# Performance work log

Hardware: AMD Instinct MI355X
Metric: run time of the kernel (lower is better)

## Reference

```python
import jax, jax.numpy as jnp
import numpy as np

N = 50000; E = 800000; IN_DIM = 128; HID = 128; OUT = 128; K_TARGET = 5000


def setup_inputs() -> dict:
    key = jax.random.key(0)
    ks = jax.random.split(key, 7)
    x = jax.random.normal(ks[0], (N, IN_DIM), jnp.float32)
    edge_index = jax.random.randint(ks[1], (2, E), 0, N, dtype=jnp.int32)
    W1 = jax.random.normal(ks[2], (IN_DIM, HID), jnp.float32) / np.float32(np.sqrt(IN_DIM))
    b1 = jnp.zeros((HID,), jnp.float32)
    W2 = jax.random.normal(ks[3], (HID, OUT), jnp.float32) / np.float32(np.sqrt(HID))
    b2 = jnp.zeros((OUT,), jnp.float32)
    w_score = jax.random.normal(ks[4], (HID,), jnp.float32) / np.float32(np.sqrt(HID))
    W_skip = jax.random.normal(ks[5], (HID, OUT), jnp.float32) / np.float32(np.sqrt(HID))
    b_skip = jnp.zeros((OUT,), jnp.float32)
    return dict(x=x, edge_index=edge_index, W1=W1, b1=b1, W2=W2, b2=b2,
                w_score=w_score, W_skip=W_skip, b_skip=b_skip)


def _gcn(h_in, row, col, W, b, nseg, edge_w=None):
    # PyG GCNConv with add_self_loops=True, normalize=True:
    # deg[i] = sum of incoming edge weights at col + 1 (self loop, weight 1)
    h = h_in @ W
    w = edge_w if edge_w is not None else jnp.ones(row.shape, h.dtype)
    deg = jax.ops.segment_sum(w, col, num_segments=nseg) + 1.0
    dinv = jax.lax.rsqrt(deg)
    norm = dinv[row] * w * dinv[col]                     # [E]
    agg = jax.ops.segment_sum(norm[:, None] * h[row], col, num_segments=nseg)
    agg = agg + (dinv * dinv)[:, None] * h               # self-loop messages
    return agg + b


def _forward(x, edge_index, W1, b1, W2, b2, w_score, W_skip, b_skip):
    row, col = edge_index[0], edge_index[1]
    n = x.shape[0]
    e = row.shape[0]
    x1 = jax.nn.relu(_gcn(x, row, col, W1, b1, n))       # conv1 + relu (dropout: eval mode)
    raw = x1 @ w_score                                    # [N]
    x1g = x1 * jnp.tanh(raw)[:, None]                     # gated features
    K = min(K_TARGET, n)
    _, kept = jax.lax.top_k(raw, K)                       # sorted desc, ties -> lower index
    keep_mask = jnp.zeros((n,), bool).at[kept].set(True)
    deg = jax.ops.segment_sum(jnp.ones((e,), jnp.int32), row, num_segments=n)  # bincount(row)
    # neighbor insertion order: edge i appends col[i] to neigh[row[i]] (order 2i),
    # then row[i] to neigh[col[i]] (order 2i+1)
    owners = jnp.concatenate([row, col])
    neighs = jnp.concatenate([col, row])
    e_ar = jnp.arange(e, dtype=jnp.int32)
    order = jnp.concatenate([2 * e_ar, 2 * e_ar + 1])
    M = 2 * e + 2
    valid = keep_mask[neighs]
    comp = deg[neighs] * M + (M - 1 - order)
    comp = jnp.where(valid, comp, -1)
    best = jax.ops.segment_max(comp, owners, num_segments=n)
    has_valid = best >= 0
    is_best = valid & (comp == best[owners])              # unique per owner (order unique)
    best_neigh = jax.ops.segment_max(jnp.where(is_best, neighs, -1), owners, num_segments=n)
    cluster_of = jnp.full((n,), -1, jnp.int32).at[kept].set(jnp.arange(K, dtype=jnp.int32))
    best_global_kept = kept[jnp.argmax(deg[kept])]
    fallback = cluster_of[best_global_kept]
    assigned = jnp.where(has_valid, cluster_of[jnp.maximum(best_neigh, 0)], fallback)
    cluster_id = jnp.where(keep_mask, cluster_of, assigned)
    # mean pool per cluster (Kc == K since kept nodes carry ids 0..K-1)
    sums = jax.ops.segment_sum(x1g, cluster_id, num_segments=K)
    counts = jnp.maximum(jax.ops.segment_sum(jnp.ones((n,), x.dtype), cluster_id, num_segments=K), 1.0)
    x_p = sums / counts[:, None]
    # coarse edges: duplicates summed == unique edges weighted by counts; self-pairs dropped
    cu, cv = cluster_id[row], cluster_id[col]
    w_e = (cu != cv).astype(x.dtype)
    x_p = _gcn(x_p, cu, cv, W2, b2, K, edge_w=w_e)        # conv2 with edge_weight
    logits = x_p[cluster_id] + x1 @ W_skip + b_skip       # broadcast up + skip
    return logits


def reference(x, edge_index, W1, b1, W2, b2, w_score, W_skip, b_skip):
    logits = _forward(x, edge_index, W1, b1, W2, b2, w_score, W_skip, b_skip)
    return (logits, 0.0)
```

## Files before the change

kernel.cpp:

```cpp
#include <hip/hip_runtime.h>
#include <cstdint>

#define N_NODES 50000
#define N_EDGES 800000
#define DIM 128
#define KSEL 5000
#define MCONST (2 * N_EDGES + 2)
#define PCH 64
#define PCH2 16
#define CANDCAP 8192
#define TM 4
#define KRB ((KSEL + 255) / 256)
#define GPERS 2048
#define DPART 16
#define DRANGE (N_NODES / DPART + 1)
#define DEB 32

typedef unsigned long long u64;
typedef uint32_t u32;

#define FMA4(A_, S_, W_) { (A_).x = fmaf((S_), (W_).x, (A_).x); (A_).y = fmaf((S_), (W_).y, (A_).y); \
                           (A_).z = fmaf((S_), (W_).z, (A_).z); (A_).w = fmaf((S_), (W_).w, (A_).w); }

__device__ __forceinline__ void gemm_tile_body(const float4* __restrict__ W4,
                                               float xs[32][DIM], float4 acc[TM],
                                               int tx, int ty) {
#pragma unroll 8
  for (int k4 = 0; k4 < 32; k4++) {
    float4 xv[TM];
#pragma unroll
    for (int m = 0; m < TM; m++) xv[m] = *(const float4*)&xs[ty + 8 * m][k4 * 4];
#pragma unroll
    for (int j = 0; j < 4; j++) {
      float4 wv = W4[(k4 * 4 + j) * 32 + tx];
#pragma unroll
      for (int m = 0; m < TM; m++) {
        float sv = (j == 0) ? xv[m].x : (j == 1) ? xv[m].y : (j == 2) ? xv[m].z : xv[m].w;
        FMA4(acc[m], sv, wv);
      }
    }
  }
}

__global__ void gemm_tiled(const float* __restrict__ X, const float* __restrict__ W,
                           float* __restrict__ Y, int nrows) {
  __shared__ float xs[32][DIM];
  int tx = threadIdx.x & 31, ty = threadIdx.x >> 5;
  int rbase = blockIdx.x * 32;
  int nval = min(32, nrows - rbase);
  const float4* X4 = (const float4*)(X + (size_t)rbase * DIM);
  float4* xs4 = (float4*)&xs[0][0];
  for (int i = threadIdx.x; i < 32 * 32; i += 256)
    if ((i >> 5) < nval) xs4[i] = X4[i];
  __syncthreads();
  float4 acc[TM];
#pragma unroll
  for (int m = 0; m < TM; m++) acc[m] = make_float4(0.f, 0.f, 0.f, 0.f);
  gemm_tile_body((const float4*)W, xs, acc, tx, ty);
#pragma unroll
  for (int m = 0; m < TM; m++) {
    int r = rbase + ty + 8 * m;
    if (r < nrows) ((float4*)(Y + (size_t)r * DIM))[tx] = acc[m];
  }
}

__global__ void gemm_tiled_div(const float* __restrict__ S, const int* __restrict__ counts,
                               const float* __restrict__ W, float* __restrict__ Y, int nrows) {
  __shared__ float xs[32][DIM];
  int tx = threadIdx.x & 31, ty = threadIdx.x >> 5;
  int rbase = blockIdx.x * 32;
  int nval = min(32, nrows - rbase);
  const float4* X4 = (const float4*)(S + (size_t)rbase * DIM);
  float4* xs4 = (float4*)&xs[0][0];
  for (int i = threadIdx.x; i < 32 * 32; i += 256) {
    int rr = i >> 5;
    if (rr < nval) {
      float inv = 1.0f / (float)max(counts[rbase + rr], 1);
      float4 v = X4[i];
      v.x *= inv; v.y *= inv; v.z *= inv; v.w *= inv;
      xs4[i] = v;
    }
  }
  __syncthreads();
  float4 acc[TM];
#pragma unroll
  for (int m = 0; m < TM; m++) acc[m] = make_float4(0.f, 0.f, 0.f, 0.f);
  gemm_tile_body((const float4*)W, xs, acc, tx, ty);
#pragma unroll
  for (int m = 0; m < TM; m++) {
    int r = rbase + ty + 8 * m;
    if (r < nrows) ((float4*)(Y + (size_t)r * DIM))[tx] = acc[m];
  }
}

__global__ void final_tiled(const float* __restrict__ x1, const float* __restrict__ Wsk,
                            const float* __restrict__ bsk, const float* __restrict__ xp2,
                            const int* __restrict__ cluster, float* __restrict__ out) {
  __shared__ float xs[32][DIM];
  int tx = threadIdx.x & 31, ty = threadIdx.x >> 5;
  int rbase = blockIdx.x * 32;
  int nval = min(32, N_NODES - rbase);
  const float4* X4 = (const float4*)(x1 + (size_t)rbase * DIM);
  float4* xs4 = (float4*)&xs[0][0];
  for (int i = threadIdx.x; i < 32 * 32; i += 256)
    if ((i >> 5) < nval) xs4[i] = X4[i];
  __syncthreads();
  float4 acc[TM];
#pragma unroll
  for (int m = 0; m < TM; m++) acc[m] = make_float4(0.f, 0.f, 0.f, 0.f);
  gemm_tile_body((const float4*)Wsk, xs, acc, tx, ty);
  float4 bv = ((const float4*)bsk)[tx];
#pragma unroll
  for (int m = 0; m < TM; m++) {
    int r = rbase + ty + 8 * m;
    if (r < N_NODES) {
      int cl = cluster[r];
      cl = (cl < 0) ? 0 : (cl >= KSEL ? KSEL - 1 : cl);
      float4 pv = ((const float4*)(xp2 + (size_t)cl * DIM))[tx];
      float4 o;
      o.x = acc[m].x + bv.x + pv.x;
      o.y = acc[m].y + bv.y + pv.y;
      o.z = acc[m].z + bv.z + pv.z;
      o.w = acc[m].w + bv.w + pv.w;
      ((float4*)(out + (size_t)r * DIM))[tx] = o;
    }
  }
  if (blockIdx.x == 0 && threadIdx.x == 0) out[(size_t)N_NODES * DIM] = 0.0f;
}

__global__ void deg_lds(const int* __restrict__ row, const int* __restrict__ col,
                        int* __restrict__ deg1, int* __restrict__ deg2) {
  __shared__ int h1[DRANGE];
  __shared__ int h2[DRANGE];
  int part = blockIdx.x >> 5;
  int eblk = blockIdx.x & 31;
  int lo = part * (N_NODES / DPART);
  int range = min(DRANGE, N_NODES - lo);
  for (int i = threadIdx.x; i < range; i += 256) { h1[i] = 0; h2[i] = 0; }
  __syncthreads();
  const int per = (N_EDGES + DEB - 1) / DEB;
  int e0 = eblk * per;
  int e1 = min(e0 + per, N_EDGES);
  for (int e = e0 + threadIdx.x; e < e1; e += 256) {
    int c = col[e] - lo;
    int r = row[e] - lo;
    if ((unsigned)c < (unsigned)(N_NODES / DPART)) atomicAdd(&h1[c], 1);
    if ((unsigned)r < (unsigned)(N_NODES / DPART)) atomicAdd(&h2[r], 1);
  }
  __syncthreads();
  int lim = min(N_NODES / DPART, N_NODES - lo);
  for (int i = threadIdx.x; i < lim; i += 256) {
    int v1 = h1[i], v2 = h2[i];
    if (v1) atomicAdd(&deg1[lo + i], v1);
    if (v2) atomicAdd(&deg2[lo + i], v2);
  }
}

__global__ void rsqrt_kernel(const int* __restrict__ deg, float* __restrict__ dinv, int n) {
  int i = blockIdx.x * blockDim.x + threadIdx.x;
  if (i < n) dinv[i] = rsqrtf((float)deg[i] + 1.0f);
}

__global__ void scan_local(const int* __restrict__ in, int* __restrict__ out,
                           int* __restrict__ bsum, float* __restrict__ dinv, int n) {
  __shared__ int s[256];
  int i = blockIdx.x * 256 + threadIdx.x;
  int v = (i < n) ? in[i] : 0;
  if (i < n) dinv[i] = rsqrtf((float)v + 1.0f);
  s[threadIdx.x] = v;
  __syncthreads();
  for (int off = 1; off < 256; off <<= 1) {
    int t = (threadIdx.x >= off) ? s[threadIdx.x - off] : 0;
    __syncthreads();
    s[threadIdx.x] += t;
    __syncthreads();
  }
  if (i < n) out[i] = s[threadIdx.x] - v;
  if (threadIdx.x == 255) bsum[blockIdx.x] = s[255];
}

__global__ void scan_bsum(int* bsum, int nb) {
  __shared__ int s[256];
  int v = (threadIdx.x < nb) ? bsum[threadIdx.x] : 0;
  s[threadIdx.x] = v;
  __syncthreads();
  for (int off = 1; off < 256; off <<= 1) {
    int t = (threadIdx.x >= off) ? s[threadIdx.x - off] : 0;
    __syncthreads();
    s[threadIdx.x] += t;
    __syncthreads();
  }
  if (threadIdx.x < nb) bsum[threadIdx.x] = s[threadIdx.x] - v;
}

__global__ void scan_add(int* out, const int* __restrict__ bsum, int n) {
  int i = blockIdx.x * 256 + threadIdx.x;
  if (i < n) out[i] += bsum[blockIdx.x];
}

__global__ void scan_small(const int* __restrict__ in, int* __restrict__ out, int n) {
  __shared__ int s[256];
  __shared__ int carry;
  if (threadIdx.x == 0) carry = 0;
  __syncthreads();
  for (int base = 0; base < n; base += 256) {
    int i = base + threadIdx.x;
    int v = (i < n) ? in[i] : 0;
    s[threadIdx.x] = v;
    __syncthreads();
    for (int off = 1; off < 256; off <<= 1) {
      int t = (threadIdx.x >= off) ? s[threadIdx.x - off] : 0;
      __syncthreads();
      s[threadIdx.x] += t;
      __syncthreads();
    }
    int c = carry;
    if (i < n) out[i] = c + s[threadIdx.x] - v;
    __syncthreads();
    if (threadIdx.x == 255) carry = c + s[255];
    __syncthreads();
  }
  if (threadIdx.x == 0) out[n] = carry;
}

__global__ void fill_ecsr(const int* __restrict__ row, const int* __restrict__ col,
                          const int* __restrict__ start, int* cursor, int* payload) {
  int e = blockIdx.x * blockDim.x + threadIdx.x;
  if (e < N_EDGES) {
    int c = col[e];
    int p = start[c] + atomicAdd(&cursor[c], 1);
    if (p >= 0 && p < N_EDGES) payload[p] = row[e];
  }
}

__global__ void fill_members(const int* __restrict__ cluster, const int* __restrict__ startn,
                             int* cursorn, int* members) {
  int i = blockIdx.x * blockDim.x + threadIdx.x;
  if (i < N_NODES) {
    int c = cluster[i];
    int p = startn[c] + atomicAdd(&cursorn[c], 1);
    if (p >= 0 && p < N_NODES) members[p] = i;
  }
}

#define GBURST4(csv_, wvl_, A0_, A1_) \
  for (; i + 3 < cnt; i += 4) { \
    int r0 = __shfl(csv_, gbase + i),     r1 = __shfl(csv_, gbase + i + 1); \
    int r2 = __shfl(csv_, gbase + i + 2), r3 = __shfl(csv_, gbase + i + 3); \
    float w0 = __shfl(wvl_, gbase + i),     w1 = __shfl(wvl_, gbase + i + 1); \
    float w2 = __shfl(wvl_, gbase + i + 2), w3 = __shfl(wvl_, gbase + i + 3); \
    float4 a0 = hb[(size_t)r0 * 32 + l32]; \
    float4 a1 = hb[(size_t)r1 * 32 + l32]; \
    float4 a2 = hb[(size_t)r2 * 32 + l32]; \
    float4 a3 = hb[(size_t)r3 * 32 + l32]; \
    FMA4(A0_, w0, a0); FMA4(A1_, w1, a1); \
    FMA4(A0_, w2, a2); FMA4(A1_, w3, a3); }

__global__ void gcn1_gather(const int* __restrict__ srcs, const int* __restrict__ start,
                            const int* __restrict__ deg1, const float* __restrict__ dinv,
                            const float* __restrict__ h, const float* __restrict__ b1,
                            const float* __restrict__ wscore,
                            float* __restrict__ B, float* __restrict__ gate,
                            u64* __restrict__ key) {
  int lane = threadIdx.x & 63;
  int g = lane >> 5, l32 = lane & 31;
  int gbase = g << 5;
  int wid = blockIdx.x * (blockDim.x >> 6) + (threadIdx.x >> 6);
  int nw = gridDim.x * (blockDim.x >> 6);
  const float4* hb = (const float4*)h;
  float4 wsv = ((const float4*)wscore)[l32];
  float4 b1v = ((const float4*)b1)[l32];
  int idxs = (l32 << 1) + g;
  int v = wid;
  if (v >= N_NODES) return;
  int s0a = start[v], na = deg1[v];
  float dia = dinv[v];
  int csvA = (idxs < na) ? srcs[s0a + idxs] : 0;
  float wvlA = (idxs < na) ? dinv[csvA] : 0.f;
  int vn = v + nw;
  int s0b = 0, nb = 0; float dib = 0.f;
  if (vn < N_NODES) { s0b = start[vn]; nb = deg1[vn]; dib = dinv[vn]; }
  while (v < N_NODES) {
    int vq = v + 2 * nw;
    int s0c = 0, nc = 0; float dic = 0.f;
    if (vq < N_NODES) { s0c = start[vq]; nc = deg1[vq]; dic = dinv[vq]; }
    int csvB = 0;
    if (vn < N_NODES && idxs < nb) csvB = srcs[s0b + idxs];
    float4 hself = hb[(size_t)v * 32 + l32];
    float4 acc0 = make_float4(0.f, 0.f, 0.f, 0.f);
    float4 acc1 = make_float4(0.f, 0.f, 0.f, 0.f);
    {
      int mm = min(64, na);
      int cnt = (mm + 1 - g) >> 1;
      int i = 0;
      GBURST4(csvA, wvlA, acc0, acc1)
      for (; i + 1 < cnt; i += 2) {
        int r0 = __shfl(csvA, gbase + i), r1 = __shfl(csvA, gbase + i + 1);
        float w0 = __shfl(wvlA, gbase + i), w1 = __shfl(wvlA, gbase + i + 1);
        float4 a0 = hb[(size_t)r0 * 32 + l32];
        float4 a1 = hb[(size_t)r1 * 32 + l32];
        FMA4(acc0, w0, a0); FMA4(acc1, w1, a1);
      }
      if (i < cnt) {
        int r0 = __shfl(csvA, gbase + i);
        float w0 = __shfl(wvlA, gbase + i);
        float4 a0 = hb[(size_t)r0 * 32 + l32];
        FMA4(acc0, w0, a0);
      }
    }
    for (int base = 64; base < na; base += 64) {
      int mm = min(64, na - base);
      int idx = base + idxs;
      int csv = (idx < na) ? srcs[s0a + idx] : 0;
      float wvl = (idx < na) ? dinv[csv] : 0.f;
      int cnt = (mm + 1 - g) >> 1;
      int i = 0;
      GBURST4(csv, wvl, acc0, acc1)
      for (; i + 1 < cnt; i += 2) {
        int r0 = __shfl(csv, gbase + i), r1 = __shfl(csv, gbase + i + 1);
        float w0 = __shfl(wvl, gbase + i), w1 = __shfl(wvl, gbase + i + 1);
        float4 a0 = hb[(size_t)r0 * 32 + l32];
        float4 a1 = hb[(size_t)r1 * 32 + l32];
        FMA4(acc0, w0, a0); FMA4(acc1, w1, a1);
      }
      if (i < cnt) {
        int r0 = __shfl(csv, gbase + i);
        float w0 = __shfl(wvl, gbase + i);
        float4 a0 = hb[(size_t)r0 * 32 + l32];
        FMA4(acc0, w0, a0);
      }
    }
    float wvlB = 0.f;
    if (vn < N_NODES && idxs < nb) wvlB = dinv[csvB];
    acc0.x += acc1.x; acc0.y += acc1.y; acc0.z += acc1.z; acc0.w += acc1.w;
    acc0.x += __shfl_xor(acc0.x, 32);
    acc0.y += __shfl_xor(acc0.y, 32);
    acc0.z += __shfl_xor(acc0.z, 32);
    acc0.w += __shfl_xor(acc0.w, 32);
    float dd = dia * dia;
    float4 vv;
    vv.x = acc0.x * dia + dd * hself.x + b1v.x;
    vv.y = acc0.y * dia + dd * hself.y + b1v.y;
    vv.z = acc0.z * dia + dd * hself.z + b1v.z;
    vv.w = acc0.w * dia + dd * hself.w + b1v.w;
    vv.x = vv.x > 0.f ? vv.x : 0.f;
    vv.y = vv.y > 0.f ? vv.y : 0.f;
    vv.z = vv.z > 0.f ? vv.z : 0.f;
    vv.w = vv.w > 0.f ? vv.w : 0.f;
    if (lane < 32) ((float4*)(B + (size_t)v * DIM))[l32] = vv;
    float sd = vv.x * wsv.x + vv.y * wsv.y + vv.z * wsv.z + vv.w * wsv.w;
    sd += __shfl_xor(sd, 1);
    sd += __shfl_xor(sd, 2);
    sd += __shfl_xor(sd, 4);
    sd += __shfl_xor(sd, 8);
    sd += __shfl_xor(sd, 16);
    if (lane == 0) {
      gate[v] = tanhf(sd);
      u32 b = __float_as_uint(sd);
      if ((b << 1) == 0u) b = 0u;
      u32 ord = (b & 0x80000000u) ? ~b : (b | 0x80000000u);
      key[v] = (((u64)(~ord)) << 32) | (u32)v;
    }
    v = vn; s0a = s0b; na = nb; dia = dib; csvA = csvB; wvlA = wvlB;
    vn = vq; s0b = s0c; nb = nc; dib = dic;
  }
}

__global__ void hist1_kernel(const u64* __restrict__ key, int* __restrict__ hist) {
  int i = blockIdx.x * blockDim.x + threadIdx.x;
  if (i < N_NODES) atomicAdd(&hist[(int)(key[i] >> 52)], 1);
}

__global__ void hist2_kernel(const u64* __restrict__ key, const int* __restrict__ selb,
                             int* __restrict__ hist) {
  int i = blockIdx.x * blockDim.x + threadIdx.x;
  if (i < N_NODES) {
    u64 k = key[i];
    if ((int)(k >> 52) == selb[0]) atomicAdd(&hist[(int)((k >> 40) & 0xFFF)], 1);
  }
}

__global__ void pick_kernel(const int* __restrict__ hist, int K_imm, int* __restrict__ selb,
                            int rem_in_slot, int bin_out_slot, int rem_out_slot) {
  __shared__ int s[256];
  int t = threadIdx.x;
  int base = t * 16;
  int loc[16];
  int sum = 0;
#pragma unroll
  for (int k = 0; k < 16; k++) { loc[k] = hist[base + k]; sum += loc[k]; }
  s[t] = sum;
  __syncthreads();
  for (int off = 1; off < 256; off <<= 1) {
    int v = (t >= off) ? s[t - off] : 0;
    __syncthreads();
    s[t] += v;
    __syncthreads();
  }
  int target = (K_imm >= 0) ? K_imm : selb[rem_in_slot];
  int prev = (t == 0) ? 0 : s[t - 1];
  if (prev < target && target <= s[t]) {
    int cum = prev;
#pragma unroll
    for (int k = 0; k < 16; k++) {
      cum += loc[k];
      if (cum >= target) {
        selb[bin_out_slot] = base + k;
        selb[rem_out_slot] = target - (cum - loc[k]);
        break;
      }
    }
  }
}

__global__ void collect_kernel(const u64* __restrict__ key, const int* __restrict__ selb,
                               u64* __restrict__ cand, int* __restrict__ ccnt) {
  int i = blockIdx.x * blockDim.x + threadIdx.x;
  if (i < N_NODES) {
    u64 k = key[i];
    if ((int)(k >> 52) == selb[0] && (int)((k >> 40) & 0xFFF) == selb[2]) {
      int p = atomicAdd(ccnt, 1);
      if (p < CANDCAP) cand[p] = k;
    }
  }
}

__global__ void thresh_kernel(const u64* __restrict__ cand, const int* __restrict__ ccnt,
                              const int* __restrict__ selb, u64* __restrict__ T) {
  int c = min(*ccnt, CANDCAP);
  int R = selb[3];
  for (int p = threadIdx.x; p < c; p += 256) {
    u64 kp = cand[p];
    int cnt = 0;
    for (int q = 0; q < c; q++) cnt += (cand[q] < kp) ? 1 : 0;
    if (cnt == R - 1) *T = kp;
  }
}

__global__ void compact_kernel(const u64* __restrict__ key, const u64* __restrict__ T,
                               int* __restrict__ krank, u64* __restrict__ kkey,
                               int* __restrict__ kidx, int* __restrict__ kcnt) {
  int i = blockIdx.x * blockDim.x + threadIdx.x;
  if (i < N_NODES) {
    krank[i] = -1;
    u64 k = key[i];
    if (k <= *T) {
      int p = atomicAdd(kcnt, 1);
      if (p < KSEL + 16) {
        kkey[p] = k;
        kidx[p] = i;
      }
    }
  }
}

__global__ void krank_count(const u64* __restrict__ kkey, int* __restrict__ rankc) {
  int p = blockIdx.x * 256 + threadIdx.x;
  u64 mykey = (p < KSEL) ? kkey[p] : ~0ull;
  int qbase = blockIdx.y * 256;
  __shared__ u64 sk[256];
  int j = qbase + threadIdx.x;
  sk[threadIdx.x] = (j < KSEL) ? kkey[j] : ~0ull;
  __syncthreads();
  int lim = min(256, KSEL - qbase);
  int cnt = 0;
#pragma unroll 8
  for (int q = 0; q < lim; q++) cnt += (sk[q] < mykey) ? 1 : 0;
  if (p < KSEL && cnt) atomicAdd(&rankc[p], cnt);
}

__global__ void krank_final(const int* __restrict__ rankc, const int* __restrict__ kidx,
                            const int* __restrict__ deg2, int* __restrict__ krank,
                            u64* fbkey) {
  int p = blockIdx.x * 256 + threadIdx.x;
  if (p < KSEL) {
    int node = kidx[p];
    if (node >= 0 && node < N_NODES) {
      int cnt = rankc[p];
      krank[node] = cnt;
      u64 fk = (((u64)(deg2[node] + 1)) << 32) | (u32)(KSEL - 1 - cnt);
      atomicMax(fbkey, fk);
    }
  }
}

__global__ void bestneigh_kernel(const int* __restrict__ row, const int* __restrict__ col,
                                 const int* __restrict__ krank, const int* __restrict__ deg2,
                                 u64* __restrict__ best) {
  int e = blockIdx.x * blockDim.x + threadIdx.x;
  if (e < N_EDGES) {
    int r = row[e], c = col[e];
    if (krank[c] >= 0) {
      u64 comp = (u64)deg2[c] * (u64)MCONST + (u64)(MCONST - 1 - 2 * e);
      atomicMax(&best[r], comp + 1);
    }
    if (krank[r] >= 0) {
      u64 comp = (u64)deg2[r] * (u64)MCONST + (u64)(MCONST - 2 - 2 * e);
      atomicMax(&best[c], comp + 1);
    }
  }
}

__global__ void assign_kernel(const int* __restrict__ krank, const u64* __restrict__ best,
                              const int* __restrict__ row, const int* __restrict__ col,
                              const u64* __restrict__ fbkey,
                              int* __restrict__ cluster, int* __restrict__ counts) {
  int i = blockIdx.x * blockDim.x + threadIdx.x;
  if (i >= N_NODES) return;
  int c;
  int rk = krank[i];
  if (rk >= 0) {
    c = rk;
  } else {
    u64 b = best[i];
    if (b > 0) {
      u64 comp = b - 1;
      int rem = (int)(comp % (u64)MCONST);
      int ord = MCONST - 1 - rem;
      int e = ord >> 1;
      int nb = (ord & 1) ? row[e] : col[e];
      c = krank[nb];
    } else {
      c = KSEL - 1 - (int)((*fbkey) & 0xffffffffu);
    }
  }
  c = (c < 0) ? 0 : (c >= KSEL ? KSEL - 1 : c);
  cluster[i] = c;
  atomicAdd(&counts[c], 1);
}

__global__ void pool_chunk(const int* __restrict__ members, const int* __restrict__ startn,
                           const int* __restrict__ cluster,
                           const float* __restrict__ x1, const float* __restrict__ gate,
                           float* __restrict__ sums) {
  int cb = blockIdx.x * PCH;
  if (cb >= N_NODES) return;
  int ce = min(cb + PCH, N_NODES);
  __shared__ int pl[PCH];
  for (int k = threadIdx.x; k < ce - cb; k += DIM) pl[k] = members[cb + k];
  __syncthreads();
  int c = cluster[pl[0]];
  int segend = startn[c + 1];
  int t = threadIdx.x;
  float acc = 0.f;
  for (int k = cb; k < ce; k++) {
    int j = pl[k - cb];
    acc = fmaf(gate[j], x1[j * DIM + t], acc);
    int k1 = k + 1;
    if (k1 == segend || k1 == ce) {
      atomicAdd(&sums[c * DIM + t], acc);
      acc = 0.f;
      if (k1 == segend && k1 < ce) {
        while (c < KSEL - 1 && startn[c + 1] <= k1) c++;
        segend = startn[c + 1];
      }
    }
  }
}

__global__ void map_csrc(const int* __restrict__ payload, const int* __restrict__ cluster,
                         int* __restrict__ csrc) {
  int p = blockIdx.x * blockDim.x + threadIdx.x;
  if (p < N_EDGES) csrc[p] = cluster[payload[p]];
}

__global__ void cdeg_kernel(const int* __restrict__ csrc, const int* __restrict__ start,
                            const int* __restrict__ deg1, const int* __restrict__ cluster,
                            int* __restrict__ degc) {
  int v = blockIdx.x * blockDim.x + threadIdx.x;
  if (v >= N_NODES) return;
  int cv = cluster[v];
  int s0 = start[v], n = deg1[v], cnt = 0;
  for (int k = 0; k < n; k++) cnt += (csrc[s0 + k] != cv) ? 1 : 0;
  if (cnt) atomicAdd(&degc[cv], cnt);
}

#define CBURST4(csv_, wvl_) \
  for (; i + 3 < cnt; i += 4) { \
    int r0 = __shfl(csv_, gbase + i),     r1 = __shfl(csv_, gbase + i + 1); \
    int r2 = __shfl(csv_, gbase + i + 2), r3 = __shfl(csv_, gbase + i + 3); \
    float w0 = __shfl(wvl_, gbase + i),     w1 = __shfl(wvl_, gbase + i + 1); \
    float w2 = __shfl(wvl_, gbase + i + 2), w3 = __shfl(wvl_, gbase + i + 3); \
    w0 = (r0 == c) ? 0.f : w0; w1 = (r1 == c) ? 0.f : w1; \
    w2 = (r2 == c) ? 0.f : w2; w3 = (r3 == c) ? 0.f : w3; \
    float4 a0 = h24[(size_t)r0 * 32 + l32]; \
    float4 a1 = h24[(size_t)r1 * 32 + l32]; \
    float4 a2 = h24[(size_t)r2 * 32 + l32]; \
    float4 a3 = h24[(size_t)r3 * 32 + l32]; \
    FMA4(acc, w0, a0); FMA4(acc, w1, a1); \
    FMA4(acc, w2, a2); FMA4(acc, w3, a3); }

__global__ void coarse_chunk(const int* __restrict__ members, const int* __restrict__ startn,
                             const int* __restrict__ cluster,
                             const int* __restrict__ start, const int* __restrict__ deg1,
                             const int* __restrict__ csrc, const float* __restrict__ dinvc,
                             const float* __restrict__ h2, float* __restrict__ agg2) {
  int cb = blockIdx.x * PCH2;
  if (cb >= N_NODES) return;
  int ce = min(cb + PCH2, N_NODES);
  int t = threadIdx.x;
  int g = t >> 5, l32 = t & 31;
  int gbase = (g & 1) << 5;
  __shared__ int pm[PCH2];
  __shared__ float red4[4][DIM];
  for (int k = t; k < ce - cb; k += 128) pm[k] = members[cb + k];
  __syncthreads();
  int c = cluster[pm[0]];
  int segend = startn[c + 1];
  const float4* h24 = (const float4*)h2;
  int idxs = (l32 << 2) + g;
  float4 acc = make_float4(0.f, 0.f, 0.f, 0.f);
  int m = cb;
  int v0 = pm[0];
  int s0a = start[v0], na = deg1[v0];
  int csvA = (idxs < na) ? csrc[s0a + idxs] : 0;
  float wvlA = dinvc[csvA];
  int s0b = 0, nb = 0;
  if (m + 1 < ce) { int v1 = pm[1]; s0b = start[v1]; nb = deg1[v1]; }
  while (m < ce) {
    int m1 = m + 1;
    int s0c = 0, nc = 0;
    if (m + 2 < ce) { int v2 = pm[m + 2 - cb]; s0c = start[v2]; nc = deg1[v2]; }
    int csvB = 0;
    if (m1 < ce && idxs < nb) csvB = csrc[s0b + idxs];
    {
      int mm = min(128, na);
      int cnt = (mm + 3 - g) >> 2;
      int i = 0;
      CBURST4(csvA, wvlA)
      for (; i < cnt; i++) {
        int r0 = __shfl(csvA, gbase + i);
        float w0 = __shfl(wvlA, gbase + i);
        w0 = (r0 == c) ? 0.f : w0;
        float4 a0 = h24[(size_t)r0 * 32 + l32];
        FMA4(acc, w0, a0);
      }
    }
    for (int base = 128; base < na; base += 128) {
      int mm = min(128, na - base);
      int idx = base + idxs;
      int csv = (idx < na) ? csrc[s0a + idx] : 0;
      float wvl = dinvc[csv];
      int cnt = (mm + 3 - g) >> 2;
      int i = 0;
      CBURST4(csv, wvl)
      for (; i < cnt; i++) {
        int r0 = __shfl(csv, gbase + i);
        float w0 = __shfl(wvl, gbase + i);
        w0 = (r0 == c) ? 0.f : w0;
        float4 a0 = h24[(size_t)r0 * 32 + l32];
        FMA4(acc, w0, a0);
      }
    }
    float wvlB = dinvc[csvB];
    if (m1 == segend || m1 == ce) {
      *(float4*)&red4[g][l32 * 4] = acc;
      __syncthreads();
      float sv = red4[0][t] + red4[1][t] + red4[2][t] + red4[3][t];
      atomicAdd(&agg2[(size_t)c * DIM + t], sv);
      __syncthreads();
      acc = make_float4(0.f, 0.f, 0.f, 0.f);
      if (m1 == segend && m1 < ce) {
        while (c < KSEL - 1 && startn[c + 1] <= m1) c++;
        segend = startn[c + 1];
      }
    }
    m = m1; s0a = s0b; na = nb; csvA = csvB; wvlA = wvlB;
    s0b = s0c; nb = nc;
  }
}

__global__ void combine2(const float* __restrict__ agg2, const float* __restrict__ h2,
                         const float* __restrict__ dinvc, const float* __restrict__ b2,
                         float* __restrict__ xp2) {
  int gid = blockIdx.x * blockDim.x + threadIdx.x;
  int c = gid >> 7, d = gid & 127;
  if (c < KSEL) {
    float dc = dinvc[c];
    xp2[gid] = agg2[gid] * dc + dc * dc * h2[gid] + b2[d];
  }
}

extern "C" void kernel_launch(void* const* d_in, const int* in_sizes, int n_in,
                              void* d_out, int out_size, void* d_ws, size_t ws_size,
                              hipStream_t stream) {
  const float* x      = (const float*)d_in[0];
  const int*   eidx   = (const int*)d_in[1];
  const float* W1     = (const float*)d_in[2];
  const float* b1     = (const float*)d_in[3];
  const float* W2     = (const float*)d_in[4];
  const float* b2     = (const float*)d_in[5];
  const float* wscore = (const float*)d_in[6];
  const float* Wsk    = (const float*)d_in[7];
  const float* bsk    = (const float*)d_in[8];
  float* out = (float*)d_out;

  const int* row = eidx;
  const int* col = eidx + N_EDGES;

  char* ws = (char*)d_ws;
#define ALIGN16(v) (((v) + 15) & ~(size_t)15)
  size_t off = 0;
#define CARVE(ptr_t, name, bytes) ptr_t name = (ptr_t)(ws + off); off = ALIGN16(off + (bytes))
  size_t h_off = off;
  CARVE(float*, h, (size_t)N_NODES * DIM * 4);
  CARVE(float*, B, (size_t)N_NODES * DIM * 4);
  CARVE(int*, payload, (size_t)N_EDGES * 4);
  CARVE(u64*, key, (size_t)N_NODES * 8);
  CARVE(float*, gate, (size_t)N_NODES * 4);
  CARVE(float*, dinv, (size_t)N_NODES * 4);
  CARVE(int*, start, (size_t)N_NODES * 4);
  CARVE(int*, bsum, 256 * 4);
  size_t zA = off;
  CARVE(int*, deg1, (size_t)N_NODES * 4);
  CARVE(int*, deg2, (size_t)N_NODES * 4);
  CARVE(int*, cursor, (size_t)N_NODES * 4);
  size_t zAsize = off - zA;

  size_t ho = h_off;
#define CARVE2(ptr_t, name, bytes) ptr_t name = (ptr_t)(ws + ho); ho = ALIGN16(ho + (bytes))
  CARVE2(int*, cluster, (size_t)N_NODES * 4);
  CARVE2(int*, members, (size_t)N_NODES * 4);
  CARVE2(int*, startn, (size_t)(KSEL + 1) * 4);
  CARVE2(float*, dinvc, (size_t)KSEL * 4);
  CARVE2(float*, h2, (size_t)KSEL * DIM * 4);
  CARVE2(int*, csrc, (size_t)N_EDGES * 4);
  size_t zB = ho;
  CARVE2(u64*, best, (size_t)N_NODES * 8);
  CARVE2(int*, counts, (size_t)KSEL * 4);
  CARVE2(int*, degc, (size_t)KSEL * 4);
  CARVE2(int*, cursorn, (size_t)KSEL * 4);
  CARVE2(float*, sums, (size_t)KSEL * DIM * 4);
  CARVE2(float*, agg2, (size_t)KSEL * DIM * 4);
  CARVE2(u64*, fbkey, 8);
  CARVE2(int*, hist1, 4096 * 4);
  CARVE2(int*, hist2, 4096 * 4);
  CARVE2(int*, rankc, (size_t)KSEL * 4);
  CARVE2(int*, ccnt, 16);
  CARVE2(int*, kcnt, 16);
  size_t zBsize = ho - zB;
  CARVE2(int*, krank, (size_t)N_NODES * 4);
  CARVE2(u64*, cand, (size_t)CANDCAP * 8);
  CARVE2(u64*, kkey, (size_t)(KSEL + 16) * 8);
  CARVE2(int*, kidx, (size_t)(KSEL + 16) * 4);
  CARVE2(int*, selb, 4 * 4);
  CARVE2(u64*, Tkey, 8);
  float* xp2 = sums;
  (void)ws_size; (void)out_size; (void)n_in; (void)in_sizes;

  const int eb  = (N_EDGES + 255) / 256;
  const int nb  = (N_NODES + 255) / 256;
  const int kbs = (KSEL + 255) / 256;
  const int pcb = (N_NODES + PCH - 1) / PCH;
  const int ccb = (N_NODES + PCH2 - 1) / PCH2;
  const int gtb = (N_NODES + 31) / 32;
  const int gkb = (KSEL + 31) / 32;

  hipMemsetAsync(ws + zA, 0, zAsize, stream);

  gemm_tiled<<<gtb, 256, 0, stream>>>(x, W1, h, N_NODES);
  deg_lds<<<DPART * DEB, 256, 0, stream>>>(row, col, deg1, deg2);
  scan_local<<<nb, 256, 0, stream>>>(deg1, start, bsum, dinv, N_NODES);
  scan_bsum<<<1, 256, 0, stream>>>(bsum, nb);
  scan_add<<<nb, 256, 0, stream>>>(start, bsum, N_NODES);
  fill_ecsr<<<eb, 256, 0, stream>>>(row, col, start, cursor, payload);
  gcn1_gather<<<GPERS, 256, 0, stream>>>(payload, start, deg1, dinv, h, b1, wscore,
                                         B, gate, key);
  hipMemsetAsync(ws + zB, 0, zBsize, stream);

  hist1_kernel<<<nb, 256, 0, stream>>>(key, hist1);
  pick_kernel<<<1, 256, 0, stream>>>(hist1, KSEL, selb, 0, 0, 1);
  hist2_kernel<<<nb, 256, 0, stream>>>(key, selb, hist2);
  pick_kernel<<<1, 256, 0, stream>>>(hist2, -1, selb, 1, 2, 3);
  collect_kernel<<<nb, 256, 0, stream>>>(key, selb, cand, ccnt);
  thresh_kernel<<<1, 256, 0, stream>>>(cand, ccnt, selb, Tkey);
  compact_kernel<<<nb, 256, 0, stream>>>(key, Tkey, krank, kkey, kidx, kcnt);
  krank_count<<<dim3(KRB, KRB), 256, 0, stream>>>(kkey, rankc);
  krank_final<<<kbs, 256, 0, stream>>>(rankc, kidx, deg2, krank, fbkey);

  bestneigh_kernel<<<eb, 256, 0, stream>>>(row, col, krank, deg2, best);
  assign_kernel<<<nb, 256, 0, stream>>>(krank, best, row, col, fbkey, cluster, counts);

  scan_small<<<1, 256, 0, stream>>>(counts, startn, KSEL);
  fill_members<<<nb, 256, 0, stream>>>(cluster, startn, cursorn, members);
  pool_chunk<<<pcb, DIM, 0, stream>>>(members, startn, cluster, B, gate, sums);
  map_csrc<<<eb, 256, 0, stream>>>(payload, cluster, csrc);
  cdeg_kernel<<<nb, 256, 0, stream>>>(csrc, start, deg1, cluster, degc);
  rsqrt_kernel<<<kbs, 256, 0, stream>>>(degc, dinvc, KSEL);

  gemm_tiled_div<<<gkb, 256, 0, stream>>>(sums, counts, W2, h2, KSEL);
  coarse_chunk<<<ccb, 128, 0, stream>>>(members, startn, cluster, start, deg1, csrc,
                                        dinvc, h2, agg2);
  combine2<<<(KSEL * DIM) / 256, 256, 0, stream>>>(agg2, h2, dinvc, b2, xp2);

  final_tiled<<<gtb, 256, 0, stream>>>(B, Wsk, bsk, xp2, cluster, out);
}
```

Baseline: 630.6 us.

## Partition CSR fill and best-neighbour max into LDS-privatized node ranges

```diff
diff --git a/kernel.cpp b/kernel.cpp
--- a/kernel.cpp
+++ b/kernel.cpp
@@ -15,6 +15,10 @@
 #define DPART 16
 #define DRANGE (N_NODES / DPART + 1)
 #define DEB 32
+#define FPART 16
+#define FRANGE (N_NODES / FPART)
+#define FCH 32
+#define FPER (N_EDGES / FCH)
 
 typedef unsigned long long u64;
 typedef uint32_t u32;
@@ -223,13 +227,50 @@
   if (threadIdx.x == 0) out[n] = carry;
 }
 
-__global__ void fill_ecsr(const int* __restrict__ row, const int* __restrict__ col,
-                          const int* __restrict__ start, int* cursor, int* payload) {
-  int e = blockIdx.x * blockDim.x + threadIdx.x;
-  if (e < N_EDGES) {
-    int c = col[e];
-    int p = start[c] + atomicAdd(&cursor[c], 1);
-    if (p >= 0 && p < N_EDGES) payload[p] = row[e];
+__global__ void fill_count(const int* __restrict__ col, int* __restrict__ chunkcnt) {
+  __shared__ int hist[FRANGE];
+  int part = blockIdx.x >> 5;
+  int ch = blockIdx.x & 31;
+  int lo = part * FRANGE;
+  for (int i = threadIdx.x; i < FRANGE; i += 256) hist[i] = 0;
+  __syncthreads();
+  int e0 = ch * FPER, e1 = min(e0 + FPER, N_EDGES);
+  for (int e = e0 + threadIdx.x; e < e1; e += 256) {
+    int c = col[e] - lo;
+    if ((unsigned)c < (unsigned)FRANGE) atomicAdd(&hist[c], 1);
+  }
+  __syncthreads();
+  for (int i = threadIdx.x; i < FRANGE; i += 256)
+    chunkcnt[(size_t)ch * N_NODES + lo + i] = hist[i];
+}
+
+__global__ void pos_scan(const int* __restrict__ start, const int* __restrict__ chunkcnt,
+                         int* __restrict__ posbase) {
+  int v = blockIdx.x * 256 + threadIdx.x;
+  if (v >= N_NODES) return;
+  int base = start[v];
+  for (int ch = 0; ch < FCH; ch++) {
+    posbase[(size_t)ch * N_NODES + v] = base;
+    base += chunkcnt[(size_t)ch * N_NODES + v];
+  }
+}
+
+__global__ void fill2(const int* __restrict__ row, const int* __restrict__ col,
+                      const int* __restrict__ posbase, int* __restrict__ payload) {
+  __shared__ int cur[FRANGE];
+  int part = blockIdx.x >> 5;
+  int ch = blockIdx.x & 31;
+  int lo = part * FRANGE;
+  for (int i = threadIdx.x; i < FRANGE; i += 256) cur[i] = 0;
+  __syncthreads();
+  int e0 = ch * FPER, e1 = min(e0 + FPER, N_EDGES);
+  for (int e = e0 + threadIdx.x; e < e1; e += 256) {
+    int c = col[e] - lo;
+    int rr = row[e];
+    if ((unsigned)c < (unsigned)FRANGE) {
+      int p = posbase[(size_t)ch * N_NODES + lo + c] + atomicAdd(&cur[c], 1);
+      if (p >= 0 && p < N_EDGES) payload[p] = rr;
+    }
   }
 }
 
@@ -484,20 +525,32 @@
   }
 }
 
-__global__ void bestneigh_kernel(const int* __restrict__ row, const int* __restrict__ col,
-                                 const int* __restrict__ krank, const int* __restrict__ deg2,
-                                 u64* __restrict__ best) {
-  int e = blockIdx.x * blockDim.x + threadIdx.x;
-  if (e < N_EDGES) {
+__global__ void bestneigh_lds(const int* __restrict__ row, const int* __restrict__ col,
+                              const int* __restrict__ krank, const int* __restrict__ deg2,
+                              u64* __restrict__ best) {
+  __shared__ u64 lmax[FRANGE];
+  int part = blockIdx.x >> 5;
+  int ch = blockIdx.x & 31;
+  int lo = part * FRANGE;
+  for (int i = threadIdx.x; i < FRANGE; i += 256) lmax[i] = 0;
+  __syncthreads();
+  int e0 = ch * FPER, e1 = min(e0 + FPER, N_EDGES);
+  for (int e = e0 + threadIdx.x; e < e1; e += 256) {
     int r = row[e], c = col[e];
-    if (krank[c] >= 0) {
+    int rl = r - lo, cl = c - lo;
+    if ((unsigned)rl < (unsigned)FRANGE && krank[c] >= 0) {
       u64 comp = (u64)deg2[c] * (u64)MCONST + (u64)(MCONST - 1 - 2 * e);
-      atomicMax(&best[r], comp + 1);
-    }
-    if (krank[r] >= 0) {
+      atomicMax(&lmax[rl], comp + 1);
+    }
+    if ((unsigned)cl < (unsigned)FRANGE && krank[r] >= 0) {
       u64 comp = (u64)deg2[r] * (u64)MCONST + (u64)(MCONST - 2 - 2 * e);
-      atomicMax(&best[c], comp + 1);
-    }
+      atomicMax(&lmax[cl], comp + 1);
+    }
+  }
+  __syncthreads();
+  for (int i = threadIdx.x; i < FRANGE; i += 256) {
+    u64 v = lmax[i];
+    if (v) atomicMax(&best[lo + i], v);
   }
 }
 
@@ -704,6 +757,7 @@
 #define CARVE(ptr_t, name, bytes) ptr_t name = (ptr_t)(ws + off); off = ALIGN16(off + (bytes))
   size_t h_off = off;
   CARVE(float*, h, (size_t)N_NODES * DIM * 4);
+  size_t B_off = off;
   CARVE(float*, B, (size_t)N_NODES * DIM * 4);
   CARVE(int*, payload, (size_t)N_EDGES * 4);
   CARVE(u64*, key, (size_t)N_NODES * 8);
@@ -716,6 +770,9 @@
   CARVE(int*, deg2, (size_t)N_NODES * 4);
   CARVE(int*, cursor, (size_t)N_NODES * 4);
   size_t zAsize = off - zA;
+
+  int* chunkcnt = (int*)(ws + B_off);
+  int* posbase  = chunkcnt + (size_t)FCH * N_NODES;
 
   size_t ho = h_off;
 #define CARVE2(ptr_t, name, bytes) ptr_t name = (ptr_t)(ws + ho); ho = ALIGN16(ho + (bytes))
@@ -746,7 +803,7 @@
   CARVE2(int*, selb, 4 * 4);
   CARVE2(u64*, Tkey, 8);
   float* xp2 = sums;
-  (void)ws_size; (void)out_size; (void)n_in; (void)in_sizes;
+  (void)ws_size; (void)out_size; (void)n_in; (void)in_sizes; (void)cursor;
 
   const int eb  = (N_EDGES + 255) / 256;
   const int nb  = (N_NODES + 255) / 256;
@@ -755,6 +812,7 @@
   const int ccb = (N_NODES + PCH2 - 1) / PCH2;
   const int gtb = (N_NODES + 31) / 32;
   const int gkb = (KSEL + 31) / 32;
+  const int fgb = FPART * FCH;
 
   hipMemsetAsync(ws + zA, 0, zAsize, stream);
 
@@ -763,7 +821,9 @@
   scan_local<<<nb, 256, 0, stream>>>(deg1, start, bsum, dinv, N_NODES);
   scan_bsum<<<1, 256, 0, stream>>>(bsum, nb);
   scan_add<<<nb, 256, 0, stream>>>(start, bsum, N_NODES);
-  fill_ecsr<<<eb, 256, 0, stream>>>(row, col, start, cursor, payload);
+  fill_count<<<fgb, 256, 0, stream>>>(col, chunkcnt);
+  pos_scan<<<nb, 256, 0, stream>>>(start, chunkcnt, posbase);
+  fill2<<<fgb, 256, 0, stream>>>(row, col, posbase, payload);
   gcn1_gather<<<GPERS, 256, 0, stream>>>(payload, start, deg1, dinv, h, b1, wscore,
                                          B, gate, key);
   hipMemsetAsync(ws + zB, 0, zBsize, stream);
@@ -778,7 +838,7 @@
   krank_count<<<dim3(KRB, KRB), 256, 0, stream>>>(kkey, rankc);
   krank_final<<<kbs, 256, 0, stream>>>(rankc, kidx, deg2, krank, fbkey);
 
-  bestneigh_kernel<<<eb, 256, 0, stream>>>(row, col, krank, deg2, best);
+  bestneigh_lds<<<fgb, 256, 0, stream>>>(row, col, krank, deg2, best);
   assign_kernel<<<nb, 256, 0, stream>>>(krank, best, row, col, fbkey, cluster, counts);
 
   scan_small<<<1, 256, 0, stream>>>(counts, startn, KSEL);
```

After: 713.6 us. 1.13x slower.
